# Kernel tuning notes

Hardware: AMD Instinct MI355X
Metric: run time of the kernel (lower is better)

## Reference

```python
import jax, jax.numpy as jnp
import numpy as np

N_NODES = 50000
N_EDGES = 800000
IN_CH, HID_CH, OUT_CH = 128, 128, 64


def setup_inputs() -> dict:
    key = jax.random.key(0)
    ks = jax.random.split(key, 8)
    x = jax.random.normal(ks[0], (N_NODES, IN_CH), dtype=jnp.float32)
    edge_index = jax.random.randint(ks[1], (2, N_EDGES), 0, N_NODES, dtype=jnp.int64)
    # PyG SAGEConv params: lin_l (applied to aggregated neighbors, has bias),
    # lin_r (applied to root node, no bias). Stored here as [in, out] matrices.
    s1 = 1.0 / np.sqrt(IN_CH)
    s2 = 1.0 / np.sqrt(HID_CH)
    W1l = jax.random.uniform(ks[2], (IN_CH, HID_CH), jnp.float32, -s1, s1)
    b1 = jnp.zeros((HID_CH,), jnp.float32)
    W1r = jax.random.uniform(ks[3], (IN_CH, HID_CH), jnp.float32, -s1, s1)
    W2l = jax.random.uniform(ks[4], (HID_CH, OUT_CH), jnp.float32, -s2, s2)
    b2 = jnp.zeros((OUT_CH,), jnp.float32)
    W2r = jax.random.uniform(ks[5], (HID_CH, OUT_CH), jnp.float32, -s2, s2)
    return {"x": x, "edge_index": edge_index, "W1l": W1l, "b1": b1,
            "W1r": W1r, "W2l": W2l, "b2": b2, "W2r": W2r}


def _sage_conv(x, src, dst, Wl, b, Wr):
    # mean-aggregate source features onto targets, then linear transform
    msg = x[src]                                        # [E, d] gather
    agg = jax.ops.segment_sum(msg, dst, num_segments=N_NODES)   # [N, d]
    deg = jax.ops.segment_sum(jnp.ones((src.shape[0],), x.dtype), dst,
                              num_segments=N_NODES)     # [N]
    mean = agg / jnp.maximum(deg, 1.0)[:, None]
    return mean @ Wl + b + x @ Wr


def reference(x, edge_index, W1l, b1, W1r, W2l, b2, W2r):
    src, dst = edge_index[0], edge_index[1]
    h = jax.nn.relu(_sage_conv(x, src, dst, W1l, b1, W1r))
    # F.dropout(p=0.3) is identity in eval mode
    return _sage_conv(h, src, dst, W2l, b2, W2r)
```

## Files before the change

### kernel.cpp

```cpp
#include <hip/hip_runtime.h>
#include <hip/hip_bf16.h>


#define TBLOCK 256
#define MAXBUCK 1024
#define HGRID 512

typedef __attribute__((ext_vector_type(8))) short short8;
typedef __attribute__((ext_vector_type(4))) float f32x4;

__device__ __forceinline__ float bf2f(ushort u) {
    union { unsigned int i; float f; } v;
    v.i = (unsigned int)u << 16;
    return v.f;
}
__device__ __forceinline__ ushort f2bf(float f) {
    union { float f; unsigned int u; } v;
    v.f = f;
    unsigned int r = v.u + 0x7fffu + ((v.u >> 16) & 1u);
    return (ushort)(r >> 16);
}

__device__ __forceinline__ int block_detect_is64(const int* __restrict__ edges) {
    __shared__ int sbad[4];
    int tid = threadIdx.x;
    int bad = 0;
    for (int i = tid; i < 2048; i += TBLOCK)
        if (edges[2 * i + 1] != 0) bad = 1;
    unsigned long long b = __ballot(bad);
    if ((tid & 63) == 0) sbad[tid >> 6] = (b != 0) ? 1 : 0;
    __syncthreads();
    int flag = (sbad[0] | sbad[1] | sbad[2] | sbad[3]) ? 0 : 1;
    __syncthreads();
    return flag;
}

__device__ __forceinline__ int load_src(const int* e, long long i, int E, int is64) {
    return is64 ? e[2 * i] : e[i];
}
__device__ __forceinline__ int load_dst(const int* e, long long i, int E, int is64) {
    return is64 ? e[2 * (long long)E + 2 * i] : e[(long long)E + i];
}

__global__ __launch_bounds__(TBLOCK) void histprep_k(
    const float* __restrict__ x,
    const float* __restrict__ W1l, const float* __restrict__ W1r,
    const float* __restrict__ W2l, const float* __restrict__ W2r,
    const int* __restrict__ edges, int E, int NBUCK,
    ushort* __restrict__ xb, ushort* __restrict__ wc1, ushort* __restrict__ wc2,
    int* __restrict__ counts, int n8, int nxb) {
    __shared__ int lh[MAXBUCK];
    const int b = blockIdx.x;
    const int t = threadIdx.x;
    if (b < HGRID) {
        const int is64 = block_detect_is64(edges);
        for (int i = t; i < NBUCK; i += TBLOCK) lh[i] = 0;
        __syncthreads();
        const int per = (E + HGRID - 1) / HGRID;
        const int b0 = b * per, b1 = min(E, b0 + per);
        for (int i = b0 + t; i < b1; i += TBLOCK)
            atomicAdd(&lh[load_dst(edges, i, E, is64) >> 8], 1);
        __syncthreads();
        for (int j = t; j < NBUCK; j += TBLOCK)
            counts[j * HGRID + b] = lh[j];
    } else {
        int pb = b - HGRID;
        if (pb < nxb) {
            int i = pb * TBLOCK + t;
            if (i >= n8) return;
            const float4* p = (const float4*)x + (size_t)i * 2;
            float4 a = p[0], bb = p[1];
            short8 o;
            o[0] = f2bf(a.x); o[1] = f2bf(a.y); o[2] = f2bf(a.z); o[3] = f2bf(a.w);
            o[4] = f2bf(bb.x); o[5] = f2bf(bb.y); o[6] = f2bf(bb.z); o[7] = f2bf(bb.w);
            *(short8*)(xb + (size_t)i * 8) = o;
        } else {
            int i = (pb - nxb) * TBLOCK + t;
            if (i < 32768) {
                int j = i & 7;
                int rest = i >> 3;
                int n = rest & 127;
                int k = ((rest >> 7) << 3) | j;
                float w = (k < 128) ? W1l[k * 128 + n] : W1r[(k - 128) * 128 + n];
                wc1[i] = f2bf(w);
            } else if (i < 49152) {
                int i2 = i - 32768;
                int j = i2 & 7;
                int rest = i2 >> 3;
                int n = rest & 127;
                int k = ((rest >> 7) << 3) | j;
                float w = (n < 64) ? W2l[k * 64 + n] : W2r[k * 64 + (n - 64)];
                wc2[i2] = f2bf(w);
            }
        }
    }
}

__global__ __launch_bounds__(TBLOCK) void scan_k(int* __restrict__ counts,
                                                 int* __restrict__ baseg, int NBUCK) {
    __shared__ int s[TBLOCK];
    const int t = threadIdx.x;
    int sum = 0;
    if (t < NBUCK) {
        const int* row = counts + (size_t)t * HGRID;
        for (int b = 0; b < HGRID; b++) sum += row[b];
    }
    s[t] = sum;
    __syncthreads();
    for (int off = 1; off < TBLOCK; off <<= 1) {
        int xv = (t >= off) ? s[t - off] : 0;
        __syncthreads();
        s[t] += xv;
        __syncthreads();
    }
    int excl = (t == 0) ? 0 : s[t - 1];
    if (t < NBUCK) {
        baseg[t] = excl;
        if (t == NBUCK - 1) baseg[NBUCK] = s[t];
        int* row = counts + (size_t)t * HGRID;
        int run = excl;
        for (int b = 0; b < HGRID; b++) {
            int c = row[b];
            row[b] = run;
            run += c;
        }
    }
}

__global__ __launch_bounds__(TBLOCK) void scatterA_k(const int* __restrict__ edges, int E,
                                                     const int* __restrict__ counts,
                                                     unsigned int* __restrict__ packed,
                                                     int NBUCK) {
    const int is64 = block_detect_is64(edges);
    __shared__ int lb[MAXBUCK];
    __shared__ int lh[MAXBUCK];
    const int b = blockIdx.x;
    const int t = threadIdx.x;
    for (int j = t; j < NBUCK; j += TBLOCK) {
        lb[j] = counts[j * HGRID + b];
        lh[j] = 0;
    }
    __syncthreads();
    const int per = (E + HGRID - 1) / HGRID;
    const int b0 = b * per, b1 = min(E, b0 + per);
    for (int i = b0 + t; i < b1; i += TBLOCK) {
        int s = load_src(edges, i, E, is64);
        int d = load_dst(edges, i, E, is64);
        int bk = d >> 8;
        int pos = lb[bk] + atomicAdd(&lh[bk], 1);
        packed[pos] = (unsigned int)s | ((unsigned int)(d & 255) << 24);
    }
}

__global__ __launch_bounds__(TBLOCK) void buildB_k(const unsigned int* __restrict__ packed,
                                                   const int* __restrict__ baseg,
                                                   int* __restrict__ offs,
                                                   int* __restrict__ degi,
                                                   float* __restrict__ invdeg,
                                                   int* __restrict__ csr, int N) {
    __shared__ int cnt[TBLOCK], scn[TBLOCK], cur[TBLOCK];
    int t = threadIdx.x;
    int bucket = blockIdx.x;
    int e0 = baseg[bucket], e1 = baseg[bucket + 1];
    cnt[t] = 0;
    cur[t] = 0;
    __syncthreads();
    for (int i = e0 + t; i < e1; i += TBLOCK)
        atomicAdd(&cnt[packed[i] >> 24], 1);
    __syncthreads();
    scn[t] = cnt[t];
    __syncthreads();
    for (int off = 1; off < TBLOCK; off <<= 1) {
        int x = (t >= off) ? scn[t - off] : 0;
        __syncthreads();
        scn[t] += x;
        __syncthreads();
    }
    int excl = (t == 0) ? 0 : scn[t - 1];
    int node = bucket * 256 + t;
    if (node < N) {
        offs[node] = e0 + excl;
        degi[node] = cnt[t];
        invdeg[node] = 1.0f / fmaxf((float)cnt[t], 1.0f);
    }
    __syncthreads();
    cnt[t] = excl;
    __syncthreads();
    for (int i = e0 + t; i < e1; i += TBLOCK) {
        unsigned int p = packed[i];
        int nl = p >> 24;
        int pos = e0 + cnt[nl] + atomicAdd(&cur[nl], 1);
        csr[pos] = (int)(p & 0xFFFFFFu);
    }
}

template <int C, bool ACCUM>
__global__ __launch_bounds__(TBLOCK) void gatherb_k(const ushort* __restrict__ feat,
                                                    const int* __restrict__ csr,
                                                    const int* __restrict__ offs,
                                                    const int* __restrict__ degi,
                                                    const float* __restrict__ invdeg,
                                                    ushort* __restrict__ outB,
                                                    float* __restrict__ outF, int N) {
    constexpr int G = C / 8;
    constexpr int NPB = TBLOCK / G;
    int n = blockIdx.x * NPB + threadIdx.x / G;
    if (n >= N) return;
    int lane = threadIdx.x % G;
    int c = lane * 8;
    int s0 = offs[n];
    int d = degi[n];
    float acc[8] = {0.f, 0.f, 0.f, 0.f, 0.f, 0.f, 0.f, 0.f};
    for (int base = 0; base < d; base += G) {
        int rem = d - base;
        int my = (lane < rem) ? csr[s0 + base + lane] : 0;
        if (rem >= G) {
#pragma unroll
            for (int j = 0; j < G; j++) {
                int s = __shfl(my, j, G);
                short8 v = *(const short8*)(feat + (size_t)s * C + c);
#pragma unroll
                for (int q = 0; q < 8; q++) acc[q] += bf2f((ushort)v[q]);
            }
        } else {
            for (int j = 0; j < rem; j++) {
                int s = __shfl(my, j, G);
                short8 v = *(const short8*)(feat + (size_t)s * C + c);
#pragma unroll
                for (int q = 0; q < 8; q++) acc[q] += bf2f((ushort)v[q]);
            }
        }
    }
    float sc = invdeg[n];
    if (ACCUM) {
        float* o = outF + (size_t)n * C + c;
        float4 p0 = *(float4*)o;
        float4 p1 = *(float4*)(o + 4);
        p0.x += sc * acc[0]; p0.y += sc * acc[1]; p0.z += sc * acc[2]; p0.w += sc * acc[3];
        p1.x += sc * acc[4]; p1.y += sc * acc[5]; p1.z += sc * acc[6]; p1.w += sc * acc[7];
        *(float4*)o = p0;
        *(float4*)(o + 4) = p1;
    } else {
        short8 o;
#pragma unroll
        for (int q = 0; q < 8; q++) o[q] = f2bf(sc * acc[q]);
        *(short8*)(outB + (size_t)n * C + c) = o;
    }
}

template <int KTOT, int EPI>
__global__ __launch_bounds__(TBLOCK) void gemm_k(const ushort* __restrict__ A0,
                                                 const ushort* __restrict__ A1,
                                                 const ushort* __restrict__ wc,
                                                 const float* __restrict__ bias,
                                                 ushort* __restrict__ outB,
                                                 float* __restrict__ outF, int N) {
    __shared__ __align__(16) ushort sW[KTOT * 128];
    for (int i = threadIdx.x * 8; i < KTOT * 128; i += TBLOCK * 8)
        *(short8*)&sW[i] = *(const short8*)&wc[i];
    __syncthreads();

    const int wave = threadIdx.x >> 6;
    const int lane = threadIdx.x & 63;
    const int quad = lane >> 4;
    const int l16 = lane & 15;
    const int m0 = (blockIdx.x * 4 + wave) * 32;
    if (m0 >= N) return;

    f32x4 acc[2][8];
#pragma unroll
    for (int t = 0; t < 2; t++)
#pragma unroll
        for (int nt = 0; nt < 8; nt++) acc[t][nt] = (f32x4){0.f, 0.f, 0.f, 0.f};

    const int k0q = quad * 8;
#pragma unroll
    for (int kb = 0; kb < KTOT; kb += 32) {
        int k = kb + k0q;
        const ushort* abase = (KTOT == 256 && k >= 128) ? (A1 + (k - 128)) : (A0 + k);
        short8 a[2];
#pragma unroll
        for (int t = 0; t < 2; t++) {
            int m = m0 + t * 16 + l16;
            if (m > N - 1) m = N - 1;
            a[t] = *(const short8*)(abase + (size_t)m * 128);
        }
#pragma unroll
        for (int nt = 0; nt < 8; nt++) {
            short8 b = *(const short8*)&sW[((k >> 3) * 128 + nt * 16 + l16) * 8];
            acc[0][nt] = __builtin_amdgcn_mfma_f32_16x16x32_bf16(a[0], b, acc[0][nt], 0, 0, 0);
            acc[1][nt] = __builtin_amdgcn_mfma_f32_16x16x32_bf16(a[1], b, acc[1][nt], 0, 0, 0);
        }
    }

#pragma unroll
    for (int t = 0; t < 2; t++) {
#pragma unroll
        for (int r = 0; r < 4; r++) {
            int m = m0 + t * 16 + quad * 4 + r;
            if (m >= N) continue;
#pragma unroll
            for (int nt = 0; nt < 8; nt++) {
                int n = nt * 16 + l16;
                float v = acc[t][nt][r];
                if (EPI == 1) {
                    v = fmaxf(v + bias[n], 0.f);
                    outB[(size_t)m * 128 + n] = f2bf(v);
                } else {
                    if (n < 64) outB[(size_t)m * 64 + n] = f2bf(v);
                    else outF[(size_t)m * 64 + (n - 64)] = v + bias[n - 64];
                }
            }
        }
    }
}

extern "C" void kernel_launch(void* const* d_in, const int* in_sizes, int n_in,
                              void* d_out, int out_size, void* d_ws, size_t ws_size,
                              hipStream_t stream) {
    const float* x = (const float*)d_in[0];
    const int* edges = (const int*)d_in[1];
    const float* W1l = (const float*)d_in[2];
    const float* b1 = (const float*)d_in[3];
    const float* W1r = (const float*)d_in[4];
    const float* W2l = (const float*)d_in[5];
    const float* b2 = (const float*)d_in[6];
    const float* W2r = (const float*)d_in[7];
    float* out = (float*)d_out;

    const int N = in_sizes[0] / 128;
    const int E = in_sizes[1] / 2;
    const int Na = (N + 63) & ~63;
    const int NBUCK = (N + 255) >> 8;
    const int n8 = N * 128 / 8;
    const int nxb = (n8 + TBLOCK - 1) / TBLOCK;

    char* WS = (char*)d_ws;
    size_t off = 0;
    auto alloc = [&](size_t bytes) {
        void* p = WS + off;
        off = (off + bytes + 255) & ~(size_t)255;
        return p;
    };
    int* counts = (int*)alloc((size_t)MAXBUCK * HGRID * 4);
    int* baseg = (int*)alloc((size_t)(MAXBUCK + 1) * 4);
    int* offs = (int*)alloc((size_t)Na * 4);
    int* degi = (int*)alloc((size_t)Na * 4);
    float* invdeg = (float*)alloc((size_t)Na * 4);
    unsigned int* packed = (unsigned int*)alloc((size_t)E * 4);
    int* csr = (int*)alloc((size_t)E * 4);
    ushort* xb = (ushort*)alloc((size_t)N * 128 * 2);
    ushort* agg1b = (ushort*)alloc((size_t)N * 128 * 2);
    ushort* hb = (ushort*)alloc((size_t)N * 128 * 2);
    ushort* t2b = (ushort*)alloc((size_t)N * 64 * 2);
    ushort* wc1 = (ushort*)alloc(32768 * 2);
    ushort* wc2 = (ushort*)alloc(16384 * 2);

    histprep_k<<<HGRID + nxb + 192, TBLOCK, 0, stream>>>(
        x, W1l, W1r, W2l, W2r, edges, E, NBUCK, xb, wc1, wc2, counts, n8, nxb);
    scan_k<<<1, TBLOCK, 0, stream>>>(counts, baseg, NBUCK);
    scatterA_k<<<HGRID, TBLOCK, 0, stream>>>(edges, E, counts, packed, NBUCK);
    buildB_k<<<NBUCK, TBLOCK, 0, stream>>>(packed, baseg, offs, degi, invdeg, csr, N);

    gatherb_k<128, false><<<(N + 15) / 16, TBLOCK, 0, stream>>>(
        xb, csr, offs, degi, invdeg, agg1b, nullptr, N);
    gemm_k<256, 1><<<(N + 127) / 128, TBLOCK, 0, stream>>>(
        agg1b, xb, wc1, b1, hb, nullptr, N);

    gemm_k<128, 2><<<(N + 127) / 128, TBLOCK, 0, stream>>>(
        hb, nullptr, wc2, b2, t2b, out, N);
    gatherb_k<64, true><<<(N + 31) / 32, TBLOCK, 0, stream>>>(
        t2b, csr, offs, degi, invdeg, nullptr, out, N);
}
```

Baseline: 231.9 us.

## Split single-block bucket scan into parallel per-bucket scan plus small global scan

The single-block scan, where each thread serially walked 512 histogram entries twice, is replaced by two kernels. One launches a block per bucket to scan its row in parallel and record the row total, and a second small kernel scans those totals into bucket bases. The scatter kernel then adds the bucket base to the local offset itself. This removes a long serial, poorly coalesced pass at the cost of one extra kernel launch.

```diff
diff --git a/kernel.cpp b/kernel.cpp
--- a/kernel.cpp
+++ b/kernel.cpp
@@ -96,16 +96,34 @@
     }
 }
 
-__global__ __launch_bounds__(TBLOCK) void scan_k(int* __restrict__ counts,
-                                                 int* __restrict__ baseg, int NBUCK) {
+__global__ __launch_bounds__(TBLOCK) void scanA_k(int* __restrict__ counts,
+                                                  int* __restrict__ total) {
+    __shared__ int s[TBLOCK];
+    const int j = blockIdx.x;
+    const int t = threadIdx.x;
+    int* row = counts + (size_t)j * HGRID;
+    int v0 = row[2 * t];
+    int v1 = row[2 * t + 1];
+    s[t] = v0 + v1;
+    __syncthreads();
+    for (int off = 1; off < TBLOCK; off <<= 1) {
+        int xv = (t >= off) ? s[t - off] : 0;
+        __syncthreads();
+        s[t] += xv;
+        __syncthreads();
+    }
+    int excl = (t == 0) ? 0 : s[t - 1];
+    row[2 * t] = excl;
+    row[2 * t + 1] = excl + v0;
+    if (t == TBLOCK - 1) total[j] = s[t];
+}
+
+__global__ __launch_bounds__(TBLOCK) void scanB_k(const int* __restrict__ total,
+                                                  int* __restrict__ baseg, int NBUCK) {
     __shared__ int s[TBLOCK];
     const int t = threadIdx.x;
-    int sum = 0;
-    if (t < NBUCK) {
-        const int* row = counts + (size_t)t * HGRID;
-        for (int b = 0; b < HGRID; b++) sum += row[b];
-    }
-    s[t] = sum;
+    int v = (t < NBUCK) ? total[t] : 0;
+    s[t] = v;
     __syncthreads();
     for (int off = 1; off < TBLOCK; off <<= 1) {
         int xv = (t >= off) ? s[t - off] : 0;
@@ -113,22 +131,15 @@
         s[t] += xv;
         __syncthreads();
     }
-    int excl = (t == 0) ? 0 : s[t - 1];
     if (t < NBUCK) {
-        baseg[t] = excl;
+        baseg[t] = (t == 0) ? 0 : s[t - 1];
         if (t == NBUCK - 1) baseg[NBUCK] = s[t];
-        int* row = counts + (size_t)t * HGRID;
-        int run = excl;
-        for (int b = 0; b < HGRID; b++) {
-            int c = row[b];
-            row[b] = run;
-            run += c;
-        }
     }
 }
 
 __global__ __launch_bounds__(TBLOCK) void scatterA_k(const int* __restrict__ edges, int E,
                                                      const int* __restrict__ counts,
+                                                     const int* __restrict__ baseg,
                                                      unsigned int* __restrict__ packed,
                                                      int NBUCK) {
     const int is64 = block_detect_is64(edges);
@@ -137,7 +148,7 @@
     const int b = blockIdx.x;
     const int t = threadIdx.x;
     for (int j = t; j < NBUCK; j += TBLOCK) {
-        lb[j] = counts[j * HGRID + b];
+        lb[j] = baseg[j] + counts[j * HGRID + b];
         lh[j] = 0;
     }
     __syncthreads();
@@ -343,6 +354,7 @@
         return p;
     };
     int* counts = (int*)alloc((size_t)MAXBUCK * HGRID * 4);
+    int* total = (int*)alloc((size_t)MAXBUCK * 4);
     int* baseg = (int*)alloc((size_t)(MAXBUCK + 1) * 4);
     int* offs = (int*)alloc((size_t)Na * 4);
     int* degi = (int*)alloc((size_t)Na * 4);
@@ -358,8 +370,9 @@
 
     histprep_k<<<HGRID + nxb + 192, TBLOCK, 0, stream>>>(
         x, W1l, W1r, W2l, W2r, edges, E, NBUCK, xb, wc1, wc2, counts, n8, nxb);
-    scan_k<<<1, TBLOCK, 0, stream>>>(counts, baseg, NBUCK);
-    scatterA_k<<<HGRID, TBLOCK, 0, stream>>>(edges, E, counts, packed, NBUCK);
+    scanA_k<<<NBUCK, TBLOCK, 0, stream>>>(counts, total);
+    scanB_k<<<1, TBLOCK, 0, stream>>>(total, baseg, NBUCK);
+    scatterA_k<<<HGRID, TBLOCK, 0, stream>>>(edges, E, counts, baseg, packed, NBUCK);
     buildB_k<<<NBUCK, TBLOCK, 0, stream>>>(packed, baseg, offs, degi, invdeg, csr, N);
 
     gatherb_k<128, false><<<(N + 15) / 16, TBLOCK, 0, stream>>>(
```

New measurement: 194.2 us. 1.19x faster.
